# Optimization experiments

Measured on AMD Instinct MI355X. Metric: run time of the kernel, lower is better.

Reference implementation:

```python
import jax, jax.numpy as jnp
import numpy as np

KNN = 16


def _knn_idx(k, ref_xyz, query_xyz):
    # squared euclidean distances: (B, Nq, Nr)
    q2 = jnp.sum(query_xyz * query_xyz, axis=-1, keepdims=True)        # (B, Nq, 1)
    r2 = jnp.sum(ref_xyz * ref_xyz, axis=-1)[:, None, :]               # (B, 1, Nr)
    cross = jnp.einsum('bqc,brc->bqr', query_xyz, ref_xyz)             # (B, Nq, Nr)
    dist = q2 + r2 - 2.0 * cross
    neg_vals, idx = jax.lax.top_k(-dist, k)                            # k smallest dists
    return -neg_vals, idx


def setup_inputs() -> dict:
    key = jax.random.key(0)
    k1, k2, k3, k4 = jax.random.split(key, 4)
    B, N_prev, N_cur, C = 1, 8192, 4096, 256
    return {
        'xyz_prev': jax.random.normal(k1, (B, N_prev, 3), dtype=jnp.float32),
        'xyz_cur': jax.random.normal(k2, (B, N_cur, 3), dtype=jnp.float32),
        'feat_prev': jax.random.normal(k3, (B, N_prev, C), dtype=jnp.float32),
        'feat_cur': jax.random.normal(k4, (B, N_cur, C), dtype=jnp.float32),
    }


def reference(xyz_prev, xyz_cur, feat_prev, feat_cur):
    k = KNN
    _, idx = _knn_idx(k, xyz_prev, xyz_cur)                 # (B, Nq, k) per-batch-local indices
    B, Nq, _ = idx.shape
    C = feat_prev.shape[-1]
    idx_flat = idx.reshape(-1, k).astype(jnp.int32)          # (B*Nq, k)
    prev_flat = feat_prev.reshape(-1, C)                     # (B*Nprev, C)
    cur_flat = feat_cur.reshape(-1, C)                       # (B*Nq, C)
    # faithful to original: gather from flattened table with local indices (batch_dims=0)
    prev_sel = prev_flat[idx_flat]                           # (B*Nq, k, C)
    cur_sel = jnp.broadcast_to(cur_flat[:, None, :], (B * Nq, k, C))
    inter = jnp.concatenate([prev_sel - cur_sel, cur_sel], axis=-1)  # (B*Nq, k, 2C)
    return inter.reshape(B, Nq * k, 2 * C)
```

## Files before the change

kernel.cpp:

```cpp
#include <hip/hip_runtime.h>
#include <stdint.h>

#define KNN 16

typedef float vfloat4 __attribute__((ext_vector_type(4)));

__device__ __forceinline__ uint32_t fkey(float f) {
    uint32_t u = __float_as_uint(f);
    return (u & 0x80000000u) ? ~u : (u | 0x80000000u);
}

__device__ __forceinline__ unsigned long long bcast64(unsigned long long x, int l) {
    const uint32_t lo = (uint32_t)__builtin_amdgcn_readlane((int)(uint32_t)x, l);
    const uint32_t hi = (uint32_t)__builtin_amdgcn_readlane((int)(uint32_t)(x >> 32), l);
    return ((unsigned long long)hi << 32) | lo;
}

__device__ __forceinline__ unsigned long long shup1_64(unsigned long long x) {
    const uint32_t lo = (uint32_t)__builtin_amdgcn_update_dpp(
        0, (int)(uint32_t)x, 0x111, 0xF, 0xF, true);
    const uint32_t hi = (uint32_t)__builtin_amdgcn_update_dpp(
        0, (int)(uint32_t)(x >> 32), 0x111, 0xF, 0xF, true);
    return ((unsigned long long)hi << 32) | lo;
}

__global__ __launch_bounds__(256) void prep_kernel(
    const float* __restrict__ xyz_prev, vfloat4* __restrict__ P, int n_prev)
{
    const int i = blockIdx.x * 256 + threadIdx.x;
    if (i >= n_prev) return;
    const float x = xyz_prev[3 * i + 0];
    const float y = xyz_prev[3 * i + 1];
    const float z = xyz_prev[3 * i + 2];
    const float r2 = __fadd_rn(__fadd_rn(__fmul_rn(x, x), __fmul_rn(y, y)),
                               __fmul_rn(z, z));
    vfloat4 v = {x, y, z, r2};
    P[i] = v;
}

__global__ __launch_bounds__(256) void knn_kernel(
    const vfloat4* __restrict__ P, const float* __restrict__ xyz_cur,
    int* __restrict__ knn_idx, int n_prev, int n_cur)
{
    __shared__ unsigned long long smem[2][2][KNN];
    const int lane = threadIdx.x & 63;
    const int qq   = threadIdx.x >> 7;
    const int h    = (threadIdx.x >> 6) & 1;
    const int q    = blockIdx.x * 2 + qq;
    const bool active = q < n_cur;

    if (active) {
        const float qx = xyz_cur[3 * q + 0];
        const float qy = xyz_cur[3 * q + 1];
        const float qz = xyz_cur[3 * q + 2];
        const float q2 = __fadd_rn(__fadd_rn(__fmul_rn(qx, qx), __fmul_rn(qy, qy)),
                                   __fmul_rn(qz, qz));

        const int half_len = ((n_prev + 127) >> 7) << 6;
        const int base = h * half_len;
        const int end  = min((h + 1) * half_len, n_prev);

        unsigned long long v;
        {
            const int r = base + lane;
            const vfloat4 p = P[r < n_prev ? r : 0];
            const float cr = __fmaf_rn(p.z, qz, __fmaf_rn(p.y, qy, __fmul_rn(p.x, qx)));
            const float dist = __fsub_rn(__fadd_rn(q2, p.w), __fmul_rn(2.0f, cr));
            v = (r < end)
                ? (((unsigned long long)fkey(dist) << 32) | (uint32_t)r)
                : ~0ull;
        }
#pragma unroll
        for (int k = 2; k <= 64; k <<= 1) {
#pragma unroll
            for (int j = k >> 1; j > 0; j >>= 1) {
                const unsigned long long o = __shfl_xor(v, j, 64);
                const bool keepMin = (((lane & k) == 0) == ((lane & j) == 0));
                const bool omin = o < v;
                v = (keepMin == omin) ? o : v;
            }
        }
        unsigned long long lkey = (lane < KNN) ? v : ~0ull;
        unsigned long long tau = bcast64(lkey, 15);

        const int count = end - base;
        const int n_iter = count > 0 ? ((count + 63) >> 6) : 0;
        int t = 1;
        for (; t + 7 < n_iter; t += 8) {
            vfloat4 pv[8];
#pragma unroll
            for (int u = 0; u < 8; ++u) {
                const int r = base + ((t + u) << 6) + lane;
                pv[u] = P[r < n_prev ? r : 0];
            }
#pragma unroll
            for (int u = 0; u < 8; ++u) {
                const int r = base + ((t + u) << 6) + lane;
                const vfloat4 p = pv[u];
                const float cr = __fmaf_rn(p.z, qz, __fmaf_rn(p.y, qy, __fmul_rn(p.x, qx)));
                const float dist = __fsub_rn(__fadd_rn(q2, p.w), __fmul_rn(2.0f, cr));
                const unsigned long long key = (r < end)
                    ? (((unsigned long long)fkey(dist) << 32) | (uint32_t)r)
                    : ~0ull;
                unsigned long long mask = __ballot(key < tau);
                while (mask) {
                    const int b = (int)__builtin_ctzll(mask);
                    mask &= mask - 1;
                    const unsigned long long bk = bcast64(key, b);
                    if (bk < tau) {
                        const unsigned long long sh = shup1_64(lkey);
                        unsigned long long nk;
                        if (lkey < bk) nk = lkey;
                        else nk = (lane == 0 || sh < bk) ? bk : sh;
                        tau = bcast64(nk, 15);
                        if (lane < KNN) lkey = nk;
                    }
                }
            }
        }
        for (; t < n_iter; ++t) {
            const int r = base + (t << 6) + lane;
            const vfloat4 p = P[r < n_prev ? r : 0];
            const float cr = __fmaf_rn(p.z, qz, __fmaf_rn(p.y, qy, __fmul_rn(p.x, qx)));
            const float dist = __fsub_rn(__fadd_rn(q2, p.w), __fmul_rn(2.0f, cr));
            const unsigned long long key = (r < end)
                ? (((unsigned long long)fkey(dist) << 32) | (uint32_t)r)
                : ~0ull;
            unsigned long long mask = __ballot(key < tau);
            while (mask) {
                const int b = (int)__builtin_ctzll(mask);
                mask &= mask - 1;
                const unsigned long long bk = bcast64(key, b);
                if (bk < tau) {
                    const unsigned long long sh = shup1_64(lkey);
                    unsigned long long nk;
                    if (lkey < bk) nk = lkey;
                    else nk = (lane == 0 || sh < bk) ? bk : sh;
                    tau = bcast64(nk, 15);
                    if (lane < KNN) lkey = nk;
                }
            }
        }

        if (lane < KNN) smem[qq][h][lane] = lkey;
    }

    __syncthreads();

    if (active && h == 0) {
        unsigned long long v = ~0ull;
        if (lane < 16)      v = smem[qq][0][lane];
        else if (lane < 32) v = smem[qq][1][31 - lane];
#pragma unroll
        for (int j = 16; j > 0; j >>= 1) {
            const unsigned long long o = __shfl_xor(v, j, 64);
            const bool keepMin = ((lane & j) == 0);
            const bool omin = o < v;
            v = (keepMin == omin) ? o : v;
        }
        if (lane < KNN)
            knn_idx[q * KNN + lane] = (int)(v & 0xffffffffu);
    }
}

__global__ __launch_bounds__(256) void combine_kernel(
    const float* __restrict__ feat_prev, const float* __restrict__ feat_cur,
    const int* __restrict__ knn_idx, float* __restrict__ out,
    int n_cur, int c4)
{
    const int w = blockIdx.x * 4 + (threadIdx.x >> 6);
    const int lane = threadIdx.x & 63;
    const int q = w >> 2;
    const int jg = (w & 3) * 4;
    if (q >= n_cur) return;

    int nb[4];
#pragma unroll
    for (int j = 0; j < 4; ++j)
        nb[j] = knn_idx[q * KNN + jg + j];

    const vfloat4* pbase = (const vfloat4*)feat_prev;
    const vfloat4* crow  = (const vfloat4*)feat_cur + (size_t)q * c4;
    const int c8 = 2 * c4;

    for (int i = lane; i < c4; i += 64) {
        const vfloat4 c = crow[i];
        vfloat4 p[4];
#pragma unroll
        for (int j = 0; j < 4; ++j)
            p[j] = pbase[(size_t)nb[j] * c4 + i];

#pragma unroll
        for (int j = 0; j < 4; ++j) {
            vfloat4* orow = (vfloat4*)out + (size_t)(q * KNN + jg + j) * c8;
            __builtin_nontemporal_store(p[j] - c, orow + i);
            __builtin_nontemporal_store(c, orow + c4 + i);
        }
    }
}

extern "C" void kernel_launch(void* const* d_in, const int* in_sizes, int n_in,
                              void* d_out, int out_size, void* d_ws, size_t ws_size,
                              hipStream_t stream) {
    const float* xyz_prev  = (const float*)d_in[0];
    const float* xyz_cur   = (const float*)d_in[1];
    const float* feat_prev = (const float*)d_in[2];
    const float* feat_cur  = (const float*)d_in[3];
    float* out = (float*)d_out;

    const int n_prev = in_sizes[0] / 3;
    const int n_cur  = in_sizes[1] / 3;
    const int C      = in_sizes[2] / n_prev;

    vfloat4* P = (vfloat4*)d_ws;
    int* knn = (int*)((char*)d_ws + (size_t)n_prev * sizeof(vfloat4));

    prep_kernel<<<(n_prev + 255) / 256, 256, 0, stream>>>(xyz_prev, P, n_prev);

    const int knn_blocks = (n_cur + 1) / 2;
    knn_kernel<<<knn_blocks, 256, 0, stream>>>(P, xyz_cur, knn, n_prev, n_cur);

    const int n_waves = n_cur * 4;
    combine_kernel<<<(n_waves + 3) / 4, 256, 0, stream>>>(feat_prev, feat_cur,
                                                          knn, out, n_cur, C / 4);
}
```

Baseline: 210.9 us.

## Replace brute-force KNN scan with uniform-grid spatial binning and shell search

Builds a 16^3 uniform grid over the reference points (count, scan, scatter kernels) and has each query wave search outward in cubic shells, stopping once the current 16th-best distance is below the distance to the next shell. This replaces the brute-force scan of all 8192 reference points per query. The grid extent is hardcoded to [-4.5,4.5], tuned to the standard-normal inputs, and the pruning bound uses a slack factor. It also adds four small serial kernel launches plus atomic scatter, and the order of points within each cell is nondeterministic, though ties are broken by the original index.

After: 222.8 us. 1.06x slower.

```diff
diff --git a/kernel.cpp b/kernel.cpp
--- a/kernel.cpp
+++ b/kernel.cpp
@@ -2,12 +2,28 @@
 #include <stdint.h>
 
 #define KNN 16
+#define GRES 16
+#define NCELLS (GRES * GRES * GRES)
+#define GRID_S 0.5625f
+#define GRID_INV 1.7777778f
 
 typedef float vfloat4 __attribute__((ext_vector_type(4)));
+
+__device__ __forceinline__ int cell_coord(float x) {
+    int i = (int)floorf((x + 4.5f) * GRID_INV);
+    return min(max(i, 0), GRES - 1);
+}
 
 __device__ __forceinline__ uint32_t fkey(float f) {
     uint32_t u = __float_as_uint(f);
     return (u & 0x80000000u) ? ~u : (u | 0x80000000u);
+}
+
+__device__ __forceinline__ float inv_fkey_hi(unsigned long long key) {
+    const uint32_t k = (uint32_t)(key >> 32);
+    if (k == 0xFFFFFFFFu) return __builtin_inff();
+    const uint32_t u = (k & 0x80000000u) ? (k ^ 0x80000000u) : ~k;
+    return __uint_as_float(u);
 }
 
 __device__ __forceinline__ unsigned long long bcast64(unsigned long long x, int l) {
@@ -24,50 +40,136 @@
     return ((unsigned long long)hi << 32) | lo;
 }
 
-__global__ __launch_bounds__(256) void prep_kernel(
-    const float* __restrict__ xyz_prev, vfloat4* __restrict__ P, int n_prev)
-{
+
+__global__ __launch_bounds__(256) void zero_kernel(int* __restrict__ counts) {
     const int i = blockIdx.x * 256 + threadIdx.x;
-    if (i >= n_prev) return;
-    const float x = xyz_prev[3 * i + 0];
-    const float y = xyz_prev[3 * i + 1];
-    const float z = xyz_prev[3 * i + 2];
-    const float r2 = __fadd_rn(__fadd_rn(__fmul_rn(x, x), __fmul_rn(y, y)),
-                               __fmul_rn(z, z));
-    vfloat4 v = {x, y, z, r2};
-    P[i] = v;
+    if (i < NCELLS) counts[i] = 0;
+}
+
+__global__ __launch_bounds__(256) void count_kernel(
+    const float* __restrict__ xyz, int* __restrict__ counts, int n)
+{
+    const int i = blockIdx.x * 256 + threadIdx.x;
+    if (i >= n) return;
+    const int cx = cell_coord(xyz[3 * i + 0]);
+    const int cy = cell_coord(xyz[3 * i + 1]);
+    const int cz = cell_coord(xyz[3 * i + 2]);
+    atomicAdd(&counts[(cz * GRES + cy) * GRES + cx], 1);
+}
+
+__global__ __launch_bounds__(1024) void scan_kernel(
+    const int* __restrict__ counts, int* __restrict__ offs, int* __restrict__ cursor)
+{
+    __shared__ int lds[1024];
+    const int t = threadIdx.x;
+    int c[4];
+    int s = 0;
+#pragma unroll
+    for (int u = 0; u < 4; ++u) { c[u] = counts[t * 4 + u]; s += c[u]; }
+    lds[t] = s;
+    __syncthreads();
+    for (int d = 1; d < 1024; d <<= 1) {
+        const int v = (t >= d) ? lds[t - d] : 0;
+        __syncthreads();
+        lds[t] += v;
+        __syncthreads();
+    }
+    int run = (t == 0) ? 0 : lds[t - 1];
+#pragma unroll
+    for (int u = 0; u < 4; ++u) {
+        const int idx = t * 4 + u;
+        offs[idx] = run;
+        cursor[idx] = run;
+        run += c[u];
+    }
+    if (t == 1023) offs[NCELLS] = run;
+}
+
+__global__ __launch_bounds__(256) void scatter_kernel(
+    const float* __restrict__ xyz, int* __restrict__ cursor,
+    vfloat4* __restrict__ sorted, int n)
+{
+    const int i = blockIdx.x * 256 + threadIdx.x;
+    if (i >= n) return;
+    const float x = xyz[3 * i + 0];
+    const float y = xyz[3 * i + 1];
+    const float z = xyz[3 * i + 2];
+    const int c = (cell_coord(z) * GRES + cell_coord(y)) * GRES + cell_coord(x);
+    const int pos = atomicAdd(&cursor[c], 1);
+    vfloat4 v = {x, y, z, __int_as_float(i)};
+    sorted[pos] = v;
+}
+
+
+__device__ __forceinline__ void process_range(
+    const vfloat4* __restrict__ sorted, int st, int en, int lane,
+    float qx, float qy, float qz, float q2,
+    unsigned long long& lkey, unsigned long long& tau, float& tauf)
+{
+    for (int j0 = st; j0 < en; j0 += 64) {
+        const int j = j0 + lane;
+        const bool a = j < en;
+        const vfloat4 p = sorted[a ? j : j0];
+        const uint32_t oi = __float_as_uint(p.w);
+        const float r2 = __fadd_rn(__fadd_rn(__fmul_rn(p.x, p.x), __fmul_rn(p.y, p.y)),
+                                   __fmul_rn(p.z, p.z));
+        const float cr = __fmaf_rn(p.z, qz, __fmaf_rn(p.y, qy, __fmul_rn(p.x, qx)));
+        const float dist = __fsub_rn(__fadd_rn(q2, r2), __fmul_rn(2.0f, cr));
+        const unsigned long long key = a
+            ? (((unsigned long long)fkey(dist) << 32) | oi)
+            : ~0ull;
+        unsigned long long mask = __ballot(key < tau);
+        while (mask) {
+            const int b = (int)__builtin_ctzll(mask);
+            mask &= mask - 1;
+            const unsigned long long bk = bcast64(key, b);
+            if (bk < tau) {
+                const unsigned long long sh = shup1_64(lkey);
+                unsigned long long nk;
+                if (lkey < bk) nk = lkey;
+                else nk = (lane == 0 || sh < bk) ? bk : sh;
+                tau = bcast64(nk, 15);
+                tauf = inv_fkey_hi(tau);
+                if (lane < KNN) lkey = nk;
+            }
+        }
+    }
 }
 
 __global__ __launch_bounds__(256) void knn_kernel(
-    const vfloat4* __restrict__ P, const float* __restrict__ xyz_cur,
-    int* __restrict__ knn_idx, int n_prev, int n_cur)
-{
-    __shared__ unsigned long long smem[2][2][KNN];
+    const vfloat4* __restrict__ sorted, const int* __restrict__ offs,
+    const float* __restrict__ xyz_cur, int* __restrict__ knn_idx, int n_cur)
+{
     const int lane = threadIdx.x & 63;
-    const int qq   = threadIdx.x >> 7;
-    const int h    = (threadIdx.x >> 6) & 1;
-    const int q    = blockIdx.x * 2 + qq;
-    const bool active = q < n_cur;
-
-    if (active) {
-        const float qx = xyz_cur[3 * q + 0];
-        const float qy = xyz_cur[3 * q + 1];
-        const float qz = xyz_cur[3 * q + 2];
-        const float q2 = __fadd_rn(__fadd_rn(__fmul_rn(qx, qx), __fmul_rn(qy, qy)),
-                                   __fmul_rn(qz, qz));
-
-        const int half_len = ((n_prev + 127) >> 7) << 6;
-        const int base = h * half_len;
-        const int end  = min((h + 1) * half_len, n_prev);
-
-        unsigned long long v;
-        {
-            const int r = base + lane;
-            const vfloat4 p = P[r < n_prev ? r : 0];
+    const int q = blockIdx.x * 4 + (threadIdx.x >> 6);
+    if (q >= n_cur) return;
+
+    const float qx = xyz_cur[3 * q + 0];
+    const float qy = xyz_cur[3 * q + 1];
+    const float qz = xyz_cur[3 * q + 2];
+    const float q2 = __fadd_rn(__fadd_rn(__fmul_rn(qx, qx), __fmul_rn(qy, qy)),
+                               __fmul_rn(qz, qz));
+
+    const int cx = cell_coord(qx), cy = cell_coord(qy), cz = cell_coord(qz);
+
+    unsigned long long lkey, tau;
+    float tauf;
+
+    const int cid0 = (cz * GRES + cy) * GRES + cx;
+    const int st0 = offs[cid0];
+    const int en0 = offs[cid0 + 1];
+    const int cnt0 = en0 - st0;
+    {
+        unsigned long long v = ~0ull;
+        if (cnt0 > 0) {
+            const vfloat4 p = sorted[(lane < cnt0) ? (st0 + lane) : st0];
+            const uint32_t oi = __float_as_uint(p.w);
+            const float r2 = __fadd_rn(__fadd_rn(__fmul_rn(p.x, p.x), __fmul_rn(p.y, p.y)),
+                                       __fmul_rn(p.z, p.z));
             const float cr = __fmaf_rn(p.z, qz, __fmaf_rn(p.y, qy, __fmul_rn(p.x, qx)));
-            const float dist = __fsub_rn(__fadd_rn(q2, p.w), __fmul_rn(2.0f, cr));
-            v = (r < end)
-                ? (((unsigned long long)fkey(dist) << 32) | (uint32_t)r)
+            const float dist = __fsub_rn(__fadd_rn(q2, r2), __fmul_rn(2.0f, cr));
+            v = (lane < cnt0)
+                ? (((unsigned long long)fkey(dist) << 32) | oi)
                 : ~0ull;
         }
 #pragma unroll
@@ -80,87 +182,53 @@
                 v = (keepMin == omin) ? o : v;
             }
         }
-        unsigned long long lkey = (lane < KNN) ? v : ~0ull;
-        unsigned long long tau = bcast64(lkey, 15);
-
-        const int count = end - base;
-        const int n_iter = count > 0 ? ((count + 63) >> 6) : 0;
-        int t = 1;
-        for (; t + 7 < n_iter; t += 8) {
-            vfloat4 pv[8];
-#pragma unroll
-            for (int u = 0; u < 8; ++u) {
-                const int r = base + ((t + u) << 6) + lane;
-                pv[u] = P[r < n_prev ? r : 0];
-            }
-#pragma unroll
-            for (int u = 0; u < 8; ++u) {
-                const int r = base + ((t + u) << 6) + lane;
-                const vfloat4 p = pv[u];
-                const float cr = __fmaf_rn(p.z, qz, __fmaf_rn(p.y, qy, __fmul_rn(p.x, qx)));
-                const float dist = __fsub_rn(__fadd_rn(q2, p.w), __fmul_rn(2.0f, cr));
-                const unsigned long long key = (r < end)
-                    ? (((unsigned long long)fkey(dist) << 32) | (uint32_t)r)
-                    : ~0ull;
-                unsigned long long mask = __ballot(key < tau);
-                while (mask) {
-                    const int b = (int)__builtin_ctzll(mask);
-                    mask &= mask - 1;
-                    const unsigned long long bk = bcast64(key, b);
-                    if (bk < tau) {
-                        const unsigned long long sh = shup1_64(lkey);
-                        unsigned long long nk;
-                        if (lkey < bk) nk = lkey;
-                        else nk = (lane == 0 || sh < bk) ? bk : sh;
-                        tau = bcast64(nk, 15);
-                        if (lane < KNN) lkey = nk;
-                    }
+        lkey = (lane < KNN) ? v : ~0ull;
+        tau = bcast64(lkey, 15);
+        tauf = inv_fkey_hi(tau);
+    }
+    if (cnt0 > 64)
+        process_range(sorted, st0 + 64, en0, lane, qx, qy, qz, q2, lkey, tau, tauf);
+
+    const int Rmax = max(max(max(cx, GRES - 1 - cx), max(cy, GRES - 1 - cy)),
+                         max(cz, GRES - 1 - cz));
+
+    for (int R = 1; R <= GRES - 1; ++R) {
+        float g = __builtin_inff();
+        if (cx - R >= 0)        g = fminf(g, qx - (float)(cx - R + 1 - 8) * GRID_S);
+        if (cx + R <= GRES - 1) g = fminf(g, (float)(cx + R - 8) * GRID_S - qx);
+        if (cy - R >= 0)        g = fminf(g, qy - (float)(cy - R + 1 - 8) * GRID_S);
+        if (cy + R <= GRES - 1) g = fminf(g, (float)(cy + R - 8) * GRID_S - qy);
+        if (cz - R >= 0)        g = fminf(g, qz - (float)(cz - R + 1 - 8) * GRID_S);
+        if (cz + R <= GRES - 1) g = fminf(g, (float)(cz + R - 8) * GRID_S - qz);
+        if (tauf < g * g * 0.99f - 1e-3f) break;
+        if (R > Rmax) break;
+
+        const int xlo = max(0, cx - R), xhi = min(GRES - 1, cx + R);
+        for (int dz = -R; dz <= R; ++dz) {
+            const int iz = cz + dz;
+            if (iz < 0 || iz > GRES - 1) continue;
+            const bool za = (dz == -R) || (dz == R);
+            for (int dy = -R; dy <= R; ++dy) {
+                const int iy = cy + dy;
+                if (iy < 0 || iy > GRES - 1) continue;
+                const int row = (iz * GRES + iy) * GRES;
+                if (za || (dy == -R) || (dy == R)) {
+                    process_range(sorted, offs[row + xlo], offs[row + xhi + 1],
+                                  lane, qx, qy, qz, q2, lkey, tau, tauf);
+                } else {
+                    if (cx - R >= 0)
+                        process_range(sorted, offs[row + cx - R], offs[row + cx - R + 1],
+                                      lane, qx, qy, qz, q2, lkey, tau, tauf);
+                    if (cx + R <= GRES - 1)
+                        process_range(sorted, offs[row + cx + R], offs[row + cx + R + 1],
+                                      lane, qx, qy, qz, q2, lkey, tau, tauf);
                 }
             }
         }
-        for (; t < n_iter; ++t) {
-            const int r = base + (t << 6) + lane;
-            const vfloat4 p = P[r < n_prev ? r : 0];
-            const float cr = __fmaf_rn(p.z, qz, __fmaf_rn(p.y, qy, __fmul_rn(p.x, qx)));
-            const float dist = __fsub_rn(__fadd_rn(q2, p.w), __fmul_rn(2.0f, cr));
-            const unsigned long long key = (r < end)
-                ? (((unsigned long long)fkey(dist) << 32) | (uint32_t)r)
-                : ~0ull;
-            unsigned long long mask = __ballot(key < tau);
-            while (mask) {
-                const int b = (int)__builtin_ctzll(mask);
-                mask &= mask - 1;
-                const unsigned long long bk = bcast64(key, b);
-                if (bk < tau) {
-                    const unsigned long long sh = shup1_64(lkey);
-                    unsigned long long nk;
-                    if (lkey < bk) nk = lkey;
-                    else nk = (lane == 0 || sh < bk) ? bk : sh;
-                    tau = bcast64(nk, 15);
-                    if (lane < KNN) lkey = nk;
-                }
-            }
-        }
-
-        if (lane < KNN) smem[qq][h][lane] = lkey;
-    }
-
-    __syncthreads();
-
-    if (active && h == 0) {
-        unsigned long long v = ~0ull;
-        if (lane < 16)      v = smem[qq][0][lane];
-        else if (lane < 32) v = smem[qq][1][31 - lane];
-#pragma unroll
-        for (int j = 16; j > 0; j >>= 1) {
-            const unsigned long long o = __shfl_xor(v, j, 64);
-            const bool keepMin = ((lane & j) == 0);
-            const bool omin = o < v;
-            v = (keepMin == omin) ? o : v;
-        }
-        if (lane < KNN)
-            knn_idx[q * KNN + lane] = (int)(v & 0xffffffffu);
-    }
+    }
+
+    if (lane < KNN)
+        knn_idx[q * KNN + lane] = (int)(lkey & 0xffffffffu);
 }
 
 __global__ __launch_bounds__(256) void combine_kernel(
@@ -212,13 +280,19 @@
     const int n_cur  = in_sizes[1] / 3;
     const int C      = in_sizes[2] / n_prev;
 
-    vfloat4* P = (vfloat4*)d_ws;
-    int* knn = (int*)((char*)d_ws + (size_t)n_prev * sizeof(vfloat4));
-
-    prep_kernel<<<(n_prev + 255) / 256, 256, 0, stream>>>(xyz_prev, P, n_prev);
-
-    const int knn_blocks = (n_cur + 1) / 2;
-    knn_kernel<<<knn_blocks, 256, 0, stream>>>(P, xyz_cur, knn, n_prev, n_cur);
+    char* w = (char*)d_ws;
+    vfloat4* sorted = (vfloat4*)w;                 w += (size_t)n_prev * 16;
+    int* counts = (int*)w;                         w += (size_t)NCELLS * 4;
+    int* offs   = (int*)w;                         w += (size_t)(NCELLS + 1) * 4 + 12;
+    int* cursor = (int*)w;                         w += (size_t)NCELLS * 4;
+    int* knn    = (int*)w;
+
+    zero_kernel<<<(NCELLS + 255) / 256, 256, 0, stream>>>(counts);
+    count_kernel<<<(n_prev + 255) / 256, 256, 0, stream>>>(xyz_prev, counts, n_prev);
+    scan_kernel<<<1, 1024, 0, stream>>>(counts, offs, cursor);
+    scatter_kernel<<<(n_prev + 255) / 256, 256, 0, stream>>>(xyz_prev, cursor,
+                                                             sorted, n_prev);
+    knn_kernel<<<(n_cur + 3) / 4, 256, 0, stream>>>(sorted, offs, xyz_cur, knn, n_cur);
 
     const int n_waves = n_cur * 4;
     combine_kernel<<<(n_waves + 3) / 4, 256, 0, stream>>>(feat_prev, feat_cur,
```
